# Performance work log

Hardware: AMD Instinct MI355X
Metric: run time of the kernel (lower is better)

Reference implementation:

```python
import jax, jax.numpy as jnp
import numpy as np

EPS = 1e-5
G, N, H, P, K = 8, 128, 64, 64, 4  # n_groups, d_state, n_heads, head_dim, conv kernel
R = H // G  # heads per group


def _rmsnorm(x, w, eps=EPS):
    return x * jax.lax.rsqrt(jnp.mean(x * x, axis=-1, keepdims=True) + eps) * w


def setup_inputs() -> dict:
    key = jax.random.key(0)
    ks = jax.random.split(key, 8)
    B, L, Dm = 2, 1024, 2048
    d_inner = 2 * Dm                      # 4096
    conv_dim = d_inner + 2 * G * N        # 6144
    proj_dim = 2 * d_inner + 2 * G * N + H  # 10304
    return {
        "hidden_states": jax.random.normal(ks[0], (B, L, Dm), jnp.float32),
        "residual": jax.random.normal(ks[1], (B, L, Dm), jnp.float32),
        "norm_w": jnp.ones((Dm,), jnp.float32),
        "in_proj_w": jax.random.normal(ks[2], (proj_dim, Dm), jnp.float32) * 0.02,
        "conv_w": jax.random.normal(ks[3], (conv_dim, K), jnp.float32) * 0.1,
        "conv_b": jnp.zeros((conv_dim,), jnp.float32),
        "A_log": jnp.log(jnp.arange(1, H + 1, dtype=jnp.float32)),
        "D_param": jnp.ones((H,), jnp.float32),
        "dt_bias": jax.random.uniform(ks[4], (H,), jnp.float32, -4.0, -1.0),
        "gate_norm_w": jnp.ones((d_inner,), jnp.float32),
        "out_proj_w": jax.random.normal(ks[5], (Dm, d_inner), jnp.float32) * 0.02,
    }


def reference(hidden_states, residual, norm_w, in_proj_w, conv_w, conv_b,
              A_log, D_param, dt_bias, gate_norm_w, out_proj_w):
    B, L, Dm = hidden_states.shape
    d_inner = 2 * Dm
    conv_dim = d_inner + 2 * G * N

    # fused residual-add RMSNorm (residual is not None branch)
    h = hidden_states + residual
    new_residual = h
    x = _rmsnorm(h, norm_w)

    # in_proj -> [z | xBC | dt]
    proj = jnp.einsum('bld,ed->ble', x, in_proj_w)
    z = proj[..., :d_inner]
    xBC = proj[..., d_inner:d_inner + conv_dim]
    dt = proj[..., d_inner + conv_dim:]            # [B, L, H]

    # causal depthwise conv1d over xBC, then SiLU
    lhs = jnp.transpose(xBC, (0, 2, 1))            # [B, C, L]
    rhs = conv_w[:, None, :]                       # [C, 1, K]
    conv = jax.lax.conv_general_dilated(
        lhs, rhs, window_strides=(1,), padding=[(K - 1, 0)],
        feature_group_count=conv_dim)
    xBC = jax.nn.silu(jnp.transpose(conv, (0, 2, 1)) + conv_b)

    xs = xBC[..., :d_inner].reshape(B, L, G, R, P)   # per-head inputs
    Bm = xBC[..., d_inner:d_inner + G * N].reshape(B, L, G, N)
    Cm = xBC[..., d_inner + G * N:].reshape(B, L, G, N)

    dt = jax.nn.softplus(dt + dt_bias)               # [B, L, H]
    A = -jnp.exp(A_log)                              # [H]
    dA = jnp.exp(dt * A).reshape(B, L, G, R)
    dtg = dt.reshape(B, L, G, R)

    # time-major for scan
    def step(hst, inp):
        dA_t, dt_t, x_t, B_t, C_t = inp            # [B,G,R], [B,G,R], [B,G,R,P], [B,G,N], [B,G,N]
        dBx = jnp.einsum('bgr,bgn,bgrp->bgrpn', dt_t, B_t, x_t)
        hst = hst * dA_t[..., None, None] + dBx    # [B,G,R,P,N]
        y_t = jnp.einsum('bgrpn,bgn->bgrp', hst, C_t)
        return hst, y_t

    tm = lambda a: jnp.moveaxis(a, 1, 0)
    h0 = jnp.zeros((B, G, R, P, N), hidden_states.dtype)
    _, ys = jax.lax.scan(step, h0, (tm(dA), tm(dtg), tm(xs), tm(Bm), tm(Cm)))
    y = jnp.moveaxis(ys, 0, 1)                     # [B, L, G, R, P]
    y = y + D_param.reshape(G, R)[None, None, :, :, None] * xs
    y = y.reshape(B, L, d_inner)

    # gated RMSNorm then out_proj
    y = _rmsnorm(y * jax.nn.silu(z), gate_norm_w)
    out = jnp.einsum('ble,de->bld', y, out_proj_w)
    return out, new_residual
```

## Files before the change

### kernel.cpp

```cpp
#include <hip/hip_runtime.h>

#define TOK 2048
#define DM 2048
#define DI 4096
#define NG 8
#define NN 128
#define PROJ_D 10304
#define PROJ_P 10496
#define CONV_D 6144
#define LSEQ 1024
#define CHUNK 64
#define NCHUNK 16

typedef unsigned short u16;
typedef __attribute__((ext_vector_type(4))) float f32x4;
typedef __attribute__((ext_vector_type(8))) short s16x8;
typedef __attribute__((ext_vector_type(4))) unsigned short u16x4;

__device__ __forceinline__ u16 f2bf(float f) {
  union { float f; unsigned u; } x; x.f = f;
  unsigned r = (x.u + 0x7FFFu + ((x.u >> 16) & 1u)) >> 16;
  return (u16)r;
}
__device__ __forceinline__ float bf2f(u16 u) {
  union { unsigned u; float f; } x; x.u = ((unsigned)u) << 16; return x.f;
}

__device__ __forceinline__ float blockReduceSum256(float s) {
  __shared__ float red[4];
  #pragma unroll
  for (int o = 32; o > 0; o >>= 1) s += __shfl_down(s, o, 64);
  int lane = threadIdx.x & 63, wid = threadIdx.x >> 6;
  if (lane == 0) red[wid] = s;
  __syncthreads();
  return red[0] + red[1] + red[2] + red[3];
}

__global__ __launch_bounds__(256) void cvt_bf16_pad(const float* __restrict__ src, u16* __restrict__ dst,
                                                    long n_src, long n_dst) {
  long i = ((long)blockIdx.x * 256 + threadIdx.x) * 4;
  if (i >= n_dst) return;
  u16x4 o;
  if (i < n_src) {
    f32x4 v = *(const f32x4*)&src[i];
    o.x = f2bf(v.x); o.y = f2bf(v.y); o.z = f2bf(v.z); o.w = f2bf(v.w);
  } else {
    o.x = 0; o.y = 0; o.z = 0; o.w = 0;
  }
  *(u16x4*)&dst[i] = o;
}

__global__ __launch_bounds__(256) void addnorm_kernel(const float* __restrict__ hs, const float* __restrict__ res,
        const float* __restrict__ w, float* __restrict__ nres, u16* __restrict__ xbf) {
  int row = blockIdx.x;
  size_t base = (size_t)row * DM;
  int tid = threadIdx.x;
  f32x4 h[2];
  float s = 0.f;
  #pragma unroll
  for (int i = 0; i < 2; i++) {
    int off = i * 1024 + tid * 4;
    f32x4 a = *(const f32x4*)&hs[base + off];
    f32x4 b = *(const f32x4*)&res[base + off];
    f32x4 v = a + b;
    h[i] = v;
    *(f32x4*)&nres[base + off] = v;
    s += v.x * v.x + v.y * v.y + v.z * v.z + v.w * v.w;
  }
  s = blockReduceSum256(s);
  float rs = rsqrtf(s * (1.f / DM) + 1e-5f);
  #pragma unroll
  for (int i = 0; i < 2; i++) {
    int off = i * 1024 + tid * 4;
    f32x4 wv = *(const f32x4*)&w[off];
    f32x4 v = h[i];
    u16x4 o;
    o.x = f2bf(v.x * rs * wv.x);
    o.y = f2bf(v.y * rs * wv.y);
    o.z = f2bf(v.z * rs * wv.z);
    o.w = f2bf(v.w * rs * wv.w);
    *(u16x4*)&xbf[base + off] = o;
  }
}

__device__ __forceinline__ void gld_lds16(const void* g, void* l) {
  __builtin_amdgcn_global_load_lds((const __attribute__((address_space(1))) void*)g,
                                   (__attribute__((address_space(3))) void*)l, 16, 0, 0);
}

__global__ __launch_bounds__(512, 4) void gemm32(const u16* __restrict__ A, const u16* __restrict__ Bw,
                                                 u16* __restrict__ C, int K, int Cstride, int nby) {
  __shared__ u16 As[3][128][32];
  __shared__ u16 Bs[3][256][32];
  int tid = threadIdx.x;
  int lane = tid & 63, w = tid >> 6;
  int wr = w >> 2, wc = w & 3;
  int cpx = gridDim.x >> 3;
  int bid = blockIdx.x;
  int lb = (bid & 7) * cpx + (bid >> 3);
  int by = lb % nby, bx = lb / nby;
  size_t m0 = (size_t)by * 128, n0 = (size_t)bx * 256;
  const u16* Ab = A + m0 * K;
  const u16* Bb = Bw + n0 * K;

  f32x4 acc[4][4];
  #pragma unroll
  for (int i = 0; i < 4; ++i)
    #pragma unroll
    for (int j = 0; j < 4; ++j) acc[i][j] = (f32x4){0.f, 0.f, 0.f, 0.f};

  int fr = lane & 15, fq = lane >> 4;
  int lrow = lane >> 2, lg = lane & 3;

  auto S = [&](int kt) {
    int bu = kt % 3;
    {
      int row = w * 16 + lrow;
      int cs = (lg ^ ((row >> 1) & 3)) * 8;
      gld_lds16(Ab + (size_t)row * K + kt * 32 + cs, &As[bu][w * 16][0]);
    }
    #pragma unroll
    for (int j = 0; j < 2; ++j) {
      int row = j * 128 + w * 16 + lrow;
      int cs = (lg ^ ((row >> 1) & 3)) * 8;
      gld_lds16(Bb + (size_t)row * K + kt * 32 + cs, &Bs[bu][j * 128 + w * 16][0]);
    }
  };

  int nkt = K >> 5;
  S(0); S(1);
  asm volatile("s_waitcnt vmcnt(3)" ::: "memory");
  __builtin_amdgcn_s_barrier();

  for (int kt = 0; kt < nkt; ++kt) {
    int bu = kt % 3;
    s16x8 a[4], b[4];
    #pragma unroll
    for (int mi = 0; mi < 4; ++mi) {
      int row = wr * 64 + mi * 16 + fr;
      a[mi] = *(const s16x8*)&As[bu][row][(fq ^ ((row >> 1) & 3)) * 8];
    }
    #pragma unroll
    for (int ni = 0; ni < 4; ++ni) {
      int row = wc * 64 + ni * 16 + fr;
      b[ni] = *(const s16x8*)&Bs[bu][row][(fq ^ ((row >> 1) & 3)) * 8];
    }
    if (kt + 2 < nkt) {
      S(kt + 2);
      asm volatile("s_waitcnt vmcnt(3)" ::: "memory");
    } else {
      asm volatile("s_waitcnt vmcnt(0)" ::: "memory");
    }
    __builtin_amdgcn_s_barrier();
    __builtin_amdgcn_s_setprio(1);
    #pragma unroll
    for (int mi = 0; mi < 4; ++mi)
      #pragma unroll
      for (int ni = 0; ni < 4; ++ni)
        acc[mi][ni] = __builtin_amdgcn_mfma_f32_16x16x32_bf16(a[mi], b[ni], acc[mi][ni], 0, 0, 0);
    __builtin_amdgcn_s_setprio(0);
    __builtin_amdgcn_s_barrier();
  }
  size_t crow0 = m0 + wr * 64 + fq * 4;
  size_t ccol0 = n0 + wc * 64 + fr;
  #pragma unroll
  for (int mi = 0; mi < 4; ++mi)
    #pragma unroll
    for (int ni = 0; ni < 4; ++ni)
      #pragma unroll
      for (int j = 0; j < 4; ++j)
        C[(crow0 + mi * 16 + j) * Cstride + ccol0 + ni * 16] = f2bf(acc[mi][ni][j]);
}

template <bool KSPLIT>
__global__ __launch_bounds__(512, 2) void gemm8p(const u16* __restrict__ A, const u16* __restrict__ Bw,
                                                 u16* __restrict__ C, int K, int Cstride, int nby,
                                                 int nks, size_t part_stride) {
  __shared__ u16 As[2][256][64];
  __shared__ u16 Bs[2][256][64];
  int tid = threadIdx.x;
  int lane = tid & 63, w = tid >> 6;
  int wr = w >> 2, wc = w & 3;
  int cpx = gridDim.x >> 3;
  int bid = blockIdx.x;
  int lb = (bid & 7) * cpx + (bid >> 3);
  int ks, by, bx;
  if constexpr (KSPLIT) {
    ks = lb % nks;
    int tile = lb / nks;
    by = tile / nby; bx = tile - by * nby;
  } else {
    ks = 0;
    by = lb % nby; bx = lb / nby;
  }
  int Ks = KSPLIT ? (K / nks) : K;
  int k0 = ks * Ks;
  size_t m0 = (size_t)by * 256, n0 = (size_t)bx * 256;
  const u16* Ab = A + m0 * K;
  const u16* Bb = Bw + n0 * K;

  f32x4 acc[8][4];
  #pragma unroll
  for (int i = 0; i < 8; ++i)
    #pragma unroll
    for (int j = 0; j < 4; ++j) acc[i][j] = (f32x4){0.f, 0.f, 0.f, 0.f};

  int l3 = lane >> 3;
  int colsw = ((lane & 7) ^ l3) << 3;
  int fr = lane & 15, fq = lane >> 4;
  int pc0 = (fq * 8) ^ ((fr & 7) << 3);
  int pc1 = pc0 ^ 32;

  auto S = [&](int kt, int mat, int half) {
    int d = kt & 1;
    const u16* src = mat ? Bb : Ab;
    u16* dstbase = mat ? &Bs[d][0][0] : &As[d][0][0];
    #pragma unroll
    for (int j = 0; j < 2; ++j) {
      int rb = half * 128 + (w * 2 + j) * 8;
      gld_lds16(src + (size_t)(rb + l3) * K + k0 + kt * 64 + colsw, dstbase + rb * 64);
    }
  };

  int nkt = Ks >> 6;
  S(0, 1, 0); S(0, 1, 1); S(0, 0, 0); S(0, 0, 1);
  S(1, 1, 0); S(1, 1, 1);
  asm volatile("s_waitcnt vmcnt(4)" ::: "memory");
  __builtin_amdgcn_s_barrier();

  for (int kt = 0; kt < nkt; ++kt) {
    int d = kt & 1;
    s16x8 b[4][2];
    #pragma unroll
    for (int q = 0; q < 4; ++q) {
      if (q == 0) {
        #pragma unroll
        for (int ni = 0; ni < 4; ++ni) {
          b[ni][0] = *(const s16x8*)&Bs[d][wc * 64 + ni * 16 + fr][pc0];
          b[ni][1] = *(const s16x8*)&Bs[d][wc * 64 + ni * 16 + fr][pc1];
        }
      }
      s16x8 a[2][2];
      #pragma unroll
      for (int mi = 0; mi < 2; ++mi) {
        a[mi][0] = *(const s16x8*)&As[d][wr * 128 + q * 32 + mi * 16 + fr][pc0];
        a[mi][1] = *(const s16x8*)&As[d][wr * 128 + q * 32 + mi * 16 + fr][pc1];
      }
      if (q == 0)      { if (kt + 1 < nkt) S(kt + 1, 0, 0); }
      else if (q == 1) { if (kt + 1 < nkt) S(kt + 1, 0, 1); }
      else if (q == 2) { if (kt + 2 < nkt) S(kt + 2, 1, 0); }
      else {
        if (kt + 2 < nkt) { S(kt + 2, 1, 1); asm volatile("s_waitcnt vmcnt(4)" ::: "memory"); }
        else              { asm volatile("s_waitcnt vmcnt(0)" ::: "memory"); }
      }
      __builtin_amdgcn_s_barrier();
      __builtin_amdgcn_s_setprio(1);
      #pragma unroll
      for (int mi = 0; mi < 2; ++mi)
        #pragma unroll
        for (int ni = 0; ni < 4; ++ni) {
          acc[q * 2 + mi][ni] = __builtin_amdgcn_mfma_f32_16x16x32_bf16(a[mi][0], b[ni][0], acc[q * 2 + mi][ni], 0, 0, 0);
          acc[q * 2 + mi][ni] = __builtin_amdgcn_mfma_f32_16x16x32_bf16(a[mi][1], b[ni][1], acc[q * 2 + mi][ni], 0, 0, 0);
        }
      __builtin_amdgcn_s_setprio(0);
      __builtin_amdgcn_s_barrier();
    }
  }
  size_t crow0 = m0 + wr * 128 + fq * 4;
  size_t ccol0 = n0 + wc * 64 + fr;
  u16* Co = KSPLIT ? (C + (size_t)ks * part_stride) : C;
  #pragma unroll
  for (int mf = 0; mf < 8; ++mf)
    #pragma unroll
    for (int ni = 0; ni < 4; ++ni)
      #pragma unroll
      for (int j = 0; j < 4; ++j)
        Co[(crow0 + mf * 16 + j) * Cstride + ccol0 + ni * 16] = f2bf(acc[mf][ni][j]);
}

__global__ __launch_bounds__(256) void reduce4_kernel(const u16* __restrict__ part, float* __restrict__ out) {
  size_t i = ((size_t)blockIdx.x * 256 + threadIdx.x) * 4;
  const size_t st = (size_t)TOK * DM;
  u16x4 p0 = *(const u16x4*)&part[i];
  u16x4 p1 = *(const u16x4*)&part[i + st];
  u16x4 p2 = *(const u16x4*)&part[i + 2 * st];
  u16x4 p3 = *(const u16x4*)&part[i + 3 * st];
  f32x4 s;
  s.x = bf2f(p0.x) + bf2f(p1.x) + bf2f(p2.x) + bf2f(p3.x);
  s.y = bf2f(p0.y) + bf2f(p1.y) + bf2f(p2.y) + bf2f(p3.y);
  s.z = bf2f(p0.z) + bf2f(p1.z) + bf2f(p2.z) + bf2f(p3.z);
  s.w = bf2f(p0.w) + bf2f(p1.w) + bf2f(p2.w) + bf2f(p3.w);
  *(f32x4*)&out[i] = s;
}

__global__ __launch_bounds__(256) void conv_silu_kernel(const u16* __restrict__ proj,
        const float* __restrict__ cw, const float* __restrict__ cb, u16* __restrict__ xbc) {
  long gid = (long)blockIdx.x * 256 + threadIdx.x;
  int c4 = (int)(gid % 1536);
  long t = gid / 1536;
  int l = (int)(t & 1023);
  int c = c4 * 4;
  const u16* base = proj + (size_t)t * PROJ_P + DI + c;
  f32x4 acc = *(const f32x4*)&cb[c];
  f32x4 w0 = *(const f32x4*)&cw[(c + 0) * 4];
  f32x4 w1 = *(const f32x4*)&cw[(c + 1) * 4];
  f32x4 w2 = *(const f32x4*)&cw[(c + 2) * 4];
  f32x4 w3 = *(const f32x4*)&cw[(c + 3) * 4];
  #pragma unroll
  for (int k = 0; k < 4; k++) {
    int ls = l - 3 + k;
    if (ls >= 0) {
      u16x4 v = *(const u16x4*)(base + ((long)(k - 3)) * PROJ_P);
      acc.x = fmaf(bf2f(v.x), w0[k], acc.x);
      acc.y = fmaf(bf2f(v.y), w1[k], acc.y);
      acc.z = fmaf(bf2f(v.z), w2[k], acc.z);
      acc.w = fmaf(bf2f(v.w), w3[k], acc.w);
    }
  }
  u16x4 o;
  o.x = f2bf(acc.x / (1.f + expf(-acc.x)));
  o.y = f2bf(acc.y / (1.f + expf(-acc.y)));
  o.z = f2bf(acc.z / (1.f + expf(-acc.z)));
  o.w = f2bf(acc.w / (1.f + expf(-acc.w)));
  *(u16x4*)&xbc[(size_t)t * CONV_D + c] = o;
}

__global__ __launch_bounds__(256) void dt_kernel(const u16* __restrict__ proj, const float* __restrict__ dt_bias,
        const float* __restrict__ A_log, float* __restrict__ dtspT, float* __restrict__ dtaT) {
  int idx = blockIdx.x * 256 + threadIdx.x;
  int t = idx >> 6, hh = idx & 63;
  int b = t >> 10, l = t & 1023;
  float dtv = bf2f(proj[(size_t)t * PROJ_P + (DI + CONV_D) + hh]) + dt_bias[hh];
  float sp = (dtv > 15.f) ? dtv : log1pf(expf(dtv));
  float Ah = -expf(A_log[hh]);
  size_t o = (size_t)(b * 64 + hh) * LSEQ + l;
  dtspT[o] = sp;
  dtaT[o] = sp * Ah;
}

__global__ __launch_bounds__(512) void ssd_kernel(const u16* __restrict__ xbc, const float* __restrict__ dtsp,
        const float* __restrict__ dta, const float* __restrict__ Dp, u16* __restrict__ y) {
  int bid = blockIdx.x;
  int g = bid & 7, b = (bid >> 3) & 1, r = (bid >> 4) & 7, ph = bid >> 7;
  int h = g * 8 + r;
  int p0 = ph * 32;
  int tid = threadIdx.x;
  int w = tid >> 6, lane = tid & 63;

  __shared__ u16 Bsh[2][64][128];
  __shared__ u16 Csh[2][64][128];
  __shared__ u16 Xt[2][32][64];
  __shared__ u16 Btw[2][128][64];
  __shared__ u16 GWsh[64][64];
  __shared__ u16 Hbf[2][32][128];
  __shared__ float dtsh[LSEQ];
  __shared__ float Lsh[LSEQ];

  const float* dtrow = dtsp + (size_t)(b * 64 + h) * LSEQ;
  const float* dtarow = dta + (size_t)(b * 64 + h) * LSEQ;
  if (tid < 256) { f32x4 v = *(const f32x4*)&dtrow[tid * 4]; *(f32x4*)&dtsh[tid * 4] = v; }
  for (int cc = w; cc < NCHUNK; cc += 8) {
    float a = dtarow[cc * 64 + lane];
    #pragma unroll
    for (int o = 1; o < 64; o <<= 1) { float t2 = __shfl_up(a, o, 64); if (lane >= o) a += t2; }
    Lsh[cc * 64 + lane] = a;
  }
  {
    u16* hp = &Hbf[0][0][0];
    for (int i = tid; i < 1024; i += 512) *(u16x4*)&hp[i * 4] = (u16x4){0, 0, 0, 0};
  }
  float Dv = Dp[h];
  const u16* xb = xbc + (size_t)b * LSEQ * CONV_D;
  int swz = (lane & 7) << 3;
  __syncthreads();

  auto stage = [&](int cc, int d) {
    int t0c = cc * 64;
    int pw = w - 4, ptid = tid - 256;
    #pragma unroll
    for (int q = 0; q < 4; ++q) {
      int rowb = pw * 16 + q * 4;
      int row = rowb + (lane >> 4);
      int colb = ((lane & 15) * 8) ^ ((row & 7) << 3);
      gld_lds16(xb + (size_t)(t0c + row) * CONV_D + DI + g * 128 + colb, &Bsh[d][rowb][0]);
      gld_lds16(xb + (size_t)(t0c + row) * CONV_D + DI + NG * NN + g * 128 + colb, &Csh[d][rowb][0]);
    }
    {
      int s = ptid & 63, pq = ptid >> 6;
      const u16* xr = xb + (size_t)(t0c + s) * CONV_D + g * 512 + r * 64 + p0;
      #pragma unroll
      for (int pb = 0; pb < 2; ++pb) {
        int pl0 = pb * 16 + pq * 4;
        u16x4 v = *(const u16x4*)&xr[pl0];
        #pragma unroll
        for (int j = 0; j < 4; ++j) {
          int p = pl0 + j;
          Xt[d][p][s ^ ((p & 7) << 3)] = v[j];
        }
      }
    }
    {
      int s = ptid & 63, nq = ptid >> 6;
      float wend = __expf(Lsh[t0c + 63] - Lsh[t0c + s]) * dtsh[t0c + s];
      const u16* br = xb + (size_t)(t0c + s) * CONV_D + DI + g * 128;
      #pragma unroll
      for (int nb = 0; nb < 8; ++nb) {
        int n0 = nb * 16 + nq * 4;
        u16x4 v = *(const u16x4*)&br[n0];
        #pragma unroll
        for (int j = 0; j < 4; ++j) {
          int n = n0 + j;
          Btw[d][n][s ^ ((n & 7) << 3)] = f2bf(bf2f(v[j]) * wend);
        }
      }
    }
  };

  if (w >= 4) stage(0, 0);
  __syncthreads();

  f32x4 hst[2][2];
  #pragma unroll
  for (int i = 0; i < 2; ++i)
    #pragma unroll
    for (int j = 0; j < 2; ++j) hst[i][j] = (f32x4){0.f, 0.f, 0.f, 0.f};

  for (int c = 0; c < NCHUNK; ++c) {
    int d = c & 1;
    int ch = c & 1;
    int t0c = c * 64;
    if (w >= 4) {
      if (c + 1 < NCHUNK) stage(c + 1, d ^ 1);
    } else {
      s16x8 aC[4];
      #pragma unroll
      for (int k = 0; k < 4; ++k)
        aC[k] = *(const s16x8*)&Csh[d][w * 16 + (lane & 15)][(k * 32 + (lane >> 4) * 8) ^ swz];
      f32x4 Gacc[4];
      #pragma unroll
      for (int st = 0; st < 4; ++st) Gacc[st] = (f32x4){0.f, 0.f, 0.f, 0.f};
      #pragma unroll
      for (int st = 0; st < 4; ++st)
        #pragma unroll
        for (int k = 0; k < 4; ++k) {
          s16x8 bB = *(const s16x8*)&Bsh[d][st * 16 + (lane & 15)][(k * 32 + (lane >> 4) * 8) ^ swz];
          Gacc[st] = __builtin_amdgcn_mfma_f32_16x16x32_bf16(aC[k], bB, Gacc[st], 0, 0, 0);
        }
      #pragma unroll
      for (int st = 0; st < 4; ++st) {
        int s = st * 16 + (lane & 15);
        float Ls = Lsh[t0c + s], dts = dtsh[t0c + s];
        #pragma unroll
        for (int j = 0; j < 4; ++j) {
          int t = w * 16 + (lane >> 4) * 4 + j;
          float wgt = (s <= t) ? __expf(Lsh[t0c + t] - Ls) * dts : 0.f;
          GWsh[t][s ^ ((t & 7) << 3)] = f2bf(Gacc[st][j] * wgt);
        }
      }
      f32x4 Yacc[2], Y2acc[2];
      #pragma unroll
      for (int pt = 0; pt < 2; ++pt) { Yacc[pt] = (f32x4){0.f,0.f,0.f,0.f}; Y2acc[pt] = (f32x4){0.f,0.f,0.f,0.f}; }
      s16x8 aGW[2];
      #pragma unroll
      for (int k = 0; k < 2; ++k)
        aGW[k] = *(const s16x8*)&GWsh[w * 16 + (lane & 15)][(k * 32 + (lane >> 4) * 8) ^ swz];
      #pragma unroll
      for (int pt = 0; pt < 2; ++pt) {
        #pragma unroll
        for (int k = 0; k < 2; ++k) {
          s16x8 bX = *(const s16x8*)&Xt[d][pt * 16 + (lane & 15)][(k * 32 + (lane >> 4) * 8) ^ swz];
          Yacc[pt] = __builtin_amdgcn_mfma_f32_16x16x32_bf16(aGW[k], bX, Yacc[pt], 0, 0, 0);
        }
        #pragma unroll
        for (int k = 0; k < 4; ++k) {
          s16x8 bH = *(const s16x8*)&Hbf[ch][pt * 16 + (lane & 15)][(k * 32 + (lane >> 4) * 8) ^ swz];
          Y2acc[pt] = __builtin_amdgcn_mfma_f32_16x16x32_bf16(aC[k], bH, Y2acc[pt], 0, 0, 0);
        }
      }
      float el[4];
      #pragma unroll
      for (int j = 0; j < 4; ++j) el[j] = __expf(Lsh[t0c + w * 16 + (lane >> 4) * 4 + j]);
      #pragma unroll
      for (int pt = 0; pt < 2; ++pt) {
        int p = pt * 16 + (lane & 15);
        #pragma unroll
        for (int j = 0; j < 4; ++j) {
          int t = w * 16 + (lane >> 4) * 4 + j;
          float xv = bf2f(Xt[d][p][t ^ ((p & 7) << 3)]);
          float yv = Yacc[pt][j] + el[j] * Y2acc[pt][j] + Dv * xv;
          y[((size_t)b * LSEQ + t0c + t) * DI + g * 512 + r * 64 + p0 + p] = f2bf(yv);
        }
      }
      float e63 = __expf(Lsh[t0c + 63]);
      s16x8 aX[2][2];
      #pragma unroll
      for (int mp = 0; mp < 2; ++mp)
        #pragma unroll
        for (int k = 0; k < 2; ++k)
          aX[mp][k] = *(const s16x8*)&Xt[d][mp * 16 + (lane & 15)][(k * 32 + (lane >> 4) * 8) ^ swz];
      #pragma unroll
      for (int mp = 0; mp < 2; ++mp)
        #pragma unroll
        for (int nn = 0; nn < 2; ++nn) {
          #pragma unroll
          for (int j = 0; j < 4; ++j) hst[mp][nn][j] *= e63;
          #pragma unroll
          for (int k = 0; k < 2; ++k) {
            s16x8 bW = *(const s16x8*)&Btw[d][w * 32 + nn * 16 + (lane & 15)][(k * 32 + (lane >> 4) * 8) ^ swz];
            hst[mp][nn] = __builtin_amdgcn_mfma_f32_16x16x32_bf16(aX[mp][k], bW, hst[mp][nn], 0, 0, 0);
          }
        }
      #pragma unroll
      for (int mp = 0; mp < 2; ++mp)
        #pragma unroll
        for (int nn = 0; nn < 2; ++nn) {
          int n = w * 32 + nn * 16 + (lane & 15);
          #pragma unroll
          for (int j = 0; j < 4; ++j) {
            int p = mp * 16 + (lane >> 4) * 4 + j;
            Hbf[ch ^ 1][p][n ^ ((p & 7) << 3)] = f2bf(hst[mp][nn][j]);
          }
        }
    }
    __syncthreads();
  }
}

__global__ __launch_bounds__(256) void gate_kernel(const u16* __restrict__ y, const u16* __restrict__ proj,
        const float* __restrict__ gw, u16* __restrict__ y2) {
  int row = blockIdx.x;
  const u16* yr = y + (size_t)row * DI;
  const u16* zr = proj + (size_t)row * PROJ_P;
  int tid = threadIdx.x;
  f32x4 v[4];
  float s = 0.f;
  #pragma unroll
  for (int i = 0; i < 4; i++) {
    int off = i * 1024 + tid * 4;
    u16x4 av = *(const u16x4*)&yr[off];
    u16x4 zv = *(const u16x4*)&zr[off];
    f32x4 t;
    float z0 = bf2f(zv.x), z1 = bf2f(zv.y), z2 = bf2f(zv.z), z3 = bf2f(zv.w);
    t.x = bf2f(av.x) * (z0 / (1.f + expf(-z0)));
    t.y = bf2f(av.y) * (z1 / (1.f + expf(-z1)));
    t.z = bf2f(av.z) * (z2 / (1.f + expf(-z2)));
    t.w = bf2f(av.w) * (z3 / (1.f + expf(-z3)));
    v[i] = t;
    s += t.x * t.x + t.y * t.y + t.z * t.z + t.w * t.w;
  }
  s = blockReduceSum256(s);
  float rs = rsqrtf(s * (1.f / DI) + 1e-5f);
  #pragma unroll
  for (int i = 0; i < 4; i++) {
    int off = i * 1024 + tid * 4;
    f32x4 wv = *(const f32x4*)&gw[off];
    u16x4 o;
    o.x = f2bf(v[i].x * rs * wv.x);
    o.y = f2bf(v[i].y * rs * wv.y);
    o.z = f2bf(v[i].z * rs * wv.z);
    o.w = f2bf(v[i].w * rs * wv.w);
    *(u16x4*)&y2[(size_t)row * DI + off] = o;
  }
}

extern "C" void kernel_launch(void* const* d_in, const int* in_sizes, int n_in,
                              void* d_out, int out_size, void* d_ws, size_t ws_size,
                              hipStream_t stream) {
  (void)in_sizes; (void)n_in; (void)out_size; (void)ws_size;
  const float* hs      = (const float*)d_in[0];
  const float* res     = (const float*)d_in[1];
  const float* norm_w  = (const float*)d_in[2];
  const float* w_in    = (const float*)d_in[3];
  const float* conv_w  = (const float*)d_in[4];
  const float* conv_b  = (const float*)d_in[5];
  const float* A_log   = (const float*)d_in[6];
  const float* D_param = (const float*)d_in[7];
  const float* dt_bias = (const float*)d_in[8];
  const float* gate_w  = (const float*)d_in[9];
  const float* w_out   = (const float*)d_in[10];

  float* out  = (float*)d_out;
  float* nres = out + (size_t)TOK * DM;

  char* ws = (char*)d_ws;
  size_t off = 0;
  u16*   WB1  = (u16*)(ws + off);   off += (size_t)PROJ_P * DM * 2;
  u16*   WB2  = (u16*)(ws + off);   off += (size_t)DM * DI * 2;
  u16*   XBF  = (u16*)(ws + off);   off += (size_t)TOK * DM * 2;
  u16*   PROJ = (u16*)(ws + off);   off += (size_t)TOK * PROJ_P * 2;
  u16*   XBC  = (u16*)(ws + off);   off += (size_t)TOK * CONV_D * 2;
  float* DTSP = (float*)(ws + off); off += (size_t)TOK * 64 * 4;
  float* DTA  = (float*)(ws + off); off += (size_t)TOK * 64 * 4;
  u16*   Y    = (u16*)(ws + off);   off += (size_t)TOK * DI * 2;
  u16*   Y2   = (u16*)(ws + off);   off += (size_t)TOK * DI * 2;
  u16*   PART = (u16*)(ws + off);   off += (size_t)4 * TOK * DM * 2;

  cvt_bf16_pad<<<20992, 256, 0, stream>>>(w_in, WB1, (long)PROJ_D * DM, (long)PROJ_P * DM);
  cvt_bf16_pad<<<8192, 256, 0, stream>>>(w_out, WB2, (long)DM * DI, (long)DM * DI);
  addnorm_kernel<<<TOK, 256, 0, stream>>>(hs, res, norm_w, nres, XBF);
  gemm32<<<(TOK / 128) * (PROJ_P / 256), 512, 0, stream>>>(XBF, WB1, PROJ, DM, PROJ_P, TOK / 128);
  conv_silu_kernel<<<(TOK * (CONV_D / 4)) / 256, 256, 0, stream>>>(PROJ, conv_w, conv_b, XBC);
  dt_kernel<<<(TOK * 64) / 256, 256, 0, stream>>>(PROJ, dt_bias, A_log, DTSP, DTA);
  ssd_kernel<<<256, 512, 0, stream>>>(XBC, DTSP, DTA, D_param, Y);
  gate_kernel<<<TOK, 256, 0, stream>>>(Y, PROJ, gate_w, Y2);
  gemm8p<true><<<(TOK / 256) * (DM / 256) * 4, 512, 0, stream>>>(Y2, WB2, PART, DI, DM, DM / 256, 4, (size_t)TOK * DM);
  reduce4_kernel<<<(TOK * DM) / 1024, 256, 0, stream>>>(PART, out);
}
```

Measured before the change: 281.9 us.

## Fuse in_proj weight fp32-to-bf16 conversion into the projection GEMM

Drops the separate conversion kernel that turned the fp32 in_proj weight into a padded bf16 copy. The GEMM now loads fp32 weight rows into registers, converts them to bf16 and writes them to LDS, double-buffered against the async A-tile loads. Rows past the real projection width are clamped on load and zeroed on write. This removes a full pass that read the fp32 weight and wrote the bf16 copy, but each weight tile is now read as fp32 by every M-block and converted there. That adds register pressure and VALU work inside the main loop.

```diff
diff --git a/kernel.cpp b/kernel.cpp
--- a/kernel.cpp
+++ b/kernel.cpp
@@ -88,10 +88,10 @@
                                    (__attribute__((address_space(3))) void*)l, 16, 0, 0);
 }
 
-__global__ __launch_bounds__(512, 4) void gemm32(const u16* __restrict__ A, const u16* __restrict__ Bw,
-                                                 u16* __restrict__ C, int K, int Cstride, int nby) {
+__global__ __launch_bounds__(512, 4) void gemm32f(const u16* __restrict__ A, const float* __restrict__ Wf,
+                                                  u16* __restrict__ C, int K, int Cstride, int nby) {
   __shared__ u16 As[3][128][32];
-  __shared__ u16 Bs[3][256][32];
+  __shared__ u16 Bs[2][256][32];
   int tid = threadIdx.x;
   int lane = tid & 63, w = tid >> 6;
   int wr = w >> 2, wc = w & 3;
@@ -101,7 +101,6 @@
   int by = lb % nby, bx = lb / nby;
   size_t m0 = (size_t)by * 128, n0 = (size_t)bx * 256;
   const u16* Ab = A + m0 * K;
-  const u16* Bb = Bw + n0 * K;
 
   f32x4 acc[4][4];
   #pragma unroll
@@ -112,28 +111,54 @@
   int fr = lane & 15, fq = lane >> 4;
   int lrow = lane >> 2, lg = lane & 3;
 
-  auto S = [&](int kt) {
+  auto SA = [&](int kt) {
     int bu = kt % 3;
-    {
-      int row = w * 16 + lrow;
-      int cs = (lg ^ ((row >> 1) & 3)) * 8;
-      gld_lds16(Ab + (size_t)row * K + kt * 32 + cs, &As[bu][w * 16][0]);
-    }
+    int row = w * 16 + lrow;
+    int cs = (lg ^ ((row >> 1) & 3)) * 8;
+    gld_lds16(Ab + (size_t)row * K + kt * 32 + cs, &As[bu][w * 16][0]);
+  };
+  auto LB = [&](int kt, f32x4 (&r)[2][2]) {
     #pragma unroll
     for (int j = 0; j < 2; ++j) {
       int row = j * 128 + w * 16 + lrow;
-      int cs = (lg ^ ((row >> 1) & 3)) * 8;
-      gld_lds16(Bb + (size_t)row * K + kt * 32 + cs, &Bs[bu][j * 128 + w * 16][0]);
+      long ng = (long)n0 + row;
+      long ngc = ng < PROJ_D ? ng : (PROJ_D - 1);
+      const float* sp = Wf + (size_t)ngc * K + kt * 32 + (lg ^ ((row >> 1) & 3)) * 8;
+      r[j][0] = *(const f32x4*)sp;
+      r[j][1] = *(const f32x4*)(sp + 4);
     }
   };
+  auto CW = [&](int kt, f32x4 (&r)[2][2]) {
+    int d = kt & 1;
+    #pragma unroll
+    for (int j = 0; j < 2; ++j) {
+      int row = j * 128 + w * 16 + lrow;
+      bool ok = ((long)n0 + row) < PROJ_D;
+      u16x4 o0, o1;
+      o0.x = ok ? f2bf(r[j][0].x) : (u16)0;
+      o0.y = ok ? f2bf(r[j][0].y) : (u16)0;
+      o0.z = ok ? f2bf(r[j][0].z) : (u16)0;
+      o0.w = ok ? f2bf(r[j][0].w) : (u16)0;
+      o1.x = ok ? f2bf(r[j][1].x) : (u16)0;
+      o1.y = ok ? f2bf(r[j][1].y) : (u16)0;
+      o1.z = ok ? f2bf(r[j][1].z) : (u16)0;
+      o1.w = ok ? f2bf(r[j][1].w) : (u16)0;
+      *(u16x4*)&Bs[d][row][lg * 8] = o0;
+      *(u16x4*)&Bs[d][row][lg * 8 + 4] = o1;
+    }
+  };
 
   int nkt = K >> 5;
-  S(0); S(1);
-  asm volatile("s_waitcnt vmcnt(3)" ::: "memory");
+  f32x4 rA[2][2], rB[2][2];
+  SA(0); LB(0, rA);
+  SA(1); LB(1, rB);
+  asm volatile("s_waitcnt vmcnt(5)" ::: "memory");
+  CW(0, rA);
+  asm volatile("s_waitcnt lgkmcnt(0)" ::: "memory");
   __builtin_amdgcn_s_barrier();
 
-  for (int kt = 0; kt < nkt; ++kt) {
-    int bu = kt % 3;
+  auto ITER = [&](int kt, f32x4 (&rload)[2][2], f32x4 (&rconv)[2][2]) {
+    int bu = kt % 3, d = kt & 1;
     s16x8 a[4], b[4];
     #pragma unroll
     for (int mi = 0; mi < 4; ++mi) {
@@ -143,14 +168,19 @@
     #pragma unroll
     for (int ni = 0; ni < 4; ++ni) {
       int row = wc * 64 + ni * 16 + fr;
-      b[ni] = *(const s16x8*)&Bs[bu][row][(fq ^ ((row >> 1) & 3)) * 8];
+      b[ni] = *(const s16x8*)&Bs[d][row][(fq ^ ((row >> 1) & 3)) * 8];
     }
     if (kt + 2 < nkt) {
-      S(kt + 2);
-      asm volatile("s_waitcnt vmcnt(3)" ::: "memory");
+      SA(kt + 2); LB(kt + 2, rload);
+      asm volatile("s_waitcnt vmcnt(5)" ::: "memory");
+      CW(kt + 1, rconv);
+    } else if (kt + 1 < nkt) {
+      asm volatile("s_waitcnt vmcnt(0)" ::: "memory");
+      CW(kt + 1, rconv);
     } else {
       asm volatile("s_waitcnt vmcnt(0)" ::: "memory");
     }
+    asm volatile("s_waitcnt lgkmcnt(0)" ::: "memory");
     __builtin_amdgcn_s_barrier();
     __builtin_amdgcn_s_setprio(1);
     #pragma unroll
@@ -160,7 +190,13 @@
         acc[mi][ni] = __builtin_amdgcn_mfma_f32_16x16x32_bf16(a[mi], b[ni], acc[mi][ni], 0, 0, 0);
     __builtin_amdgcn_s_setprio(0);
     __builtin_amdgcn_s_barrier();
-  }
+  };
+
+  for (int kt = 0; kt < nkt; kt += 2) {
+    ITER(kt,     rA, rB);
+    ITER(kt + 1, rB, rA);
+  }
+
   size_t crow0 = m0 + wr * 64 + fq * 4;
   size_t ccol0 = n0 + wc * 64 + fr;
   #pragma unroll
@@ -584,7 +620,6 @@
 
   char* ws = (char*)d_ws;
   size_t off = 0;
-  u16*   WB1  = (u16*)(ws + off);   off += (size_t)PROJ_P * DM * 2;
   u16*   WB2  = (u16*)(ws + off);   off += (size_t)DM * DI * 2;
   u16*   XBF  = (u16*)(ws + off);   off += (size_t)TOK * DM * 2;
   u16*   PROJ = (u16*)(ws + off);   off += (size_t)TOK * PROJ_P * 2;
@@ -595,10 +630,9 @@
   u16*   Y2   = (u16*)(ws + off);   off += (size_t)TOK * DI * 2;
   u16*   PART = (u16*)(ws + off);   off += (size_t)4 * TOK * DM * 2;
 
-  cvt_bf16_pad<<<20992, 256, 0, stream>>>(w_in, WB1, (long)PROJ_D * DM, (long)PROJ_P * DM);
   cvt_bf16_pad<<<8192, 256, 0, stream>>>(w_out, WB2, (long)DM * DI, (long)DM * DI);
   addnorm_kernel<<<TOK, 256, 0, stream>>>(hs, res, norm_w, nres, XBF);
-  gemm32<<<(TOK / 128) * (PROJ_P / 256), 512, 0, stream>>>(XBF, WB1, PROJ, DM, PROJ_P, TOK / 128);
+  gemm32f<<<(TOK / 128) * (PROJ_P / 256), 512, 0, stream>>>(XBF, w_in, PROJ, DM, PROJ_P, TOK / 128);
   conv_silu_kernel<<<(TOK * (CONV_D / 4)) / 256, 256, 0, stream>>>(PROJ, conv_w, conv_b, XBC);
   dt_kernel<<<(TOK * 64) / 256, 256, 0, stream>>>(PROJ, dt_bias, A_log, DTSP, DTA);
   ssd_kernel<<<256, 512, 0, stream>>>(XBC, DTSP, DTA, D_param, Y);
```

After: 921.5 us. 227% more time.
